# Kernel tuning notes

Measured on AMD Instinct MI355X. Metric: run time of the kernel, lower is better.

Reference implementation:

```python
import jax, jax.numpy as jnp
import numpy as np

B, N, D, H = 8, 1024, 768, 12
HD = D // H  # head_dim = 64


def setup_inputs() -> dict:
    key = jax.random.key(0)
    ks = jax.random.split(key, 7)
    s = 1.0 / np.sqrt(D)  # xavier-ish scale for weights
    return {
        "x1": jax.random.normal(ks[0], (B, N, D), dtype=jnp.float32),
        "x2": jax.random.normal(ks[1], (B, N, D), dtype=jnp.float32),
        "Wq": jax.random.normal(ks[2], (D, D), dtype=jnp.float32) * s,
        "Wk": jax.random.normal(ks[3], (D, D), dtype=jnp.float32) * s,
        "Wv": jax.random.normal(ks[4], (D, D), dtype=jnp.float32) * s,
        "Wo": jax.random.normal(ks[5], (D, D), dtype=jnp.float32) * s,
        "bo": jnp.zeros((D,), dtype=jnp.float32),
    }


def _heads(x):
    # (B, N, D) -> (B, H, N, HD)
    return x.reshape(B, -1, H, HD).transpose(0, 2, 1, 3)


def reference(x1, x2, Wq, Wk, Wv, Wo, bo):
    scale = 1.0 / jnp.sqrt(jnp.asarray(HD, x1.dtype))
    q1 = _heads(x1 @ Wq.T)               # (B,H,N,HD)
    k1 = _heads(x1 @ Wk.T)
    v1 = _heads(x1 @ Wv.T)
    k2 = _heads(x2 @ Wk.T)
    v2 = _heads(x2 @ Wv.T)
    kc = jnp.concatenate([k1, k2], axis=2)   # (B,H,2N,HD)
    vc = jnp.concatenate([v1, v2], axis=2)
    attn = jnp.einsum('bhnd,bhmd->bhnm', q1, kc) * scale  # (B,H,N,2N)
    attn = jax.nn.softmax(attn, axis=-1)
    out = jnp.einsum('bhnm,bhmd->bhnd', attn, vc)          # (B,H,N,HD)
    out = out.transpose(0, 2, 1, 3).reshape(B, N, D)
    return out @ Wo.T + bo
```

## Files before the change

### kernel.cpp

```cpp
#include <hip/hip_runtime.h>


typedef __bf16 bf16x8 __attribute__((ext_vector_type(8)));
typedef float  f32x4  __attribute__((ext_vector_type(4)));
typedef unsigned int u32x4 __attribute__((ext_vector_type(4)));
typedef short  s16x4  __attribute__((ext_vector_type(4)));
typedef short  s16x8  __attribute__((ext_vector_type(8)));

__device__ __forceinline__ unsigned short bf16bits(float f) {
    return __builtin_bit_cast(unsigned short, (__bf16)f);
}
__device__ __forceinline__ unsigned pk2(float a, float b) {
    return (unsigned)bf16bits(a) | ((unsigned)bf16bits(b) << 16);
}
__device__ __forceinline__ bf16x8 asbf(u32x4 v) {
    return __builtin_bit_cast(bf16x8, v);
}
__device__ __forceinline__ float fexp2(float x) {
#if __has_builtin(__builtin_amdgcn_exp2f)
    return __builtin_amdgcn_exp2f(x);
#else
    return exp2f(x);
#endif
}
__device__ __forceinline__ float frcp(float x) {
#if __has_builtin(__builtin_amdgcn_rcpf)
    return __builtin_amdgcn_rcpf(x);
#else
    return 1.0f / x;
#endif
}

#define MFMA32(a, b, c) __builtin_amdgcn_mfma_f32_16x16x32_bf16((a), (b), (c), 0, 0, 0)

__global__ __launch_bounds__(256) void convert_all(
    const float* __restrict__ x1, const float* __restrict__ x2,
    const float* __restrict__ Wq, const float* __restrict__ Wk,
    const float* __restrict__ Wv, const float* __restrict__ Wo,
    unsigned short* __restrict__ x1b, unsigned short* __restrict__ x2b,
    unsigned short* __restrict__ Wcat, unsigned short* __restrict__ Wob)
{
    const float* src; unsigned short* dst; int n4;
    switch (blockIdx.y) {
        case 0:  src = x1; dst = x1b;            n4 = 1572864; break;
        case 1:  src = x2; dst = x2b;            n4 = 1572864; break;
        case 2:  src = Wq; dst = Wcat;           n4 = 147456;  break;
        case 3:  src = Wk; dst = Wcat +  589824; n4 = 147456;  break;
        case 4:  src = Wv; dst = Wcat + 1179648; n4 = 147456;  break;
        default: src = Wo; dst = Wob;            n4 = 147456;  break;
    }
    int i = blockIdx.x * 256 + threadIdx.x;
    if (i >= n4) return;
    float4 v = ((const float4*)src)[i];
    unsigned* o32 = (unsigned*)(dst + (size_t)i * 4);
    o32[0] = pk2(v.x, v.y);
    o32[1] = pk2(v.z, v.w);
}

template<int MODE>
__global__ __launch_bounds__(256) void gemm_qkv(
    const unsigned short* __restrict__ A1, const unsigned short* __restrict__ A2,
    const unsigned short* __restrict__ Wcat,
    unsigned short* __restrict__ dQ, unsigned short* __restrict__ dK,
    unsigned short* __restrict__ dV, float* __restrict__ dO,
    const float* __restrict__ bias)
{
    __shared__ u32x4 smA[2048];
    __shared__ u32x4 smB[2048];

    const int tid  = threadIdx.x;
    const int lane = tid & 63;
    const int l15  = lane & 15;
    const int g    = lane >> 4;
    const int wid  = tid >> 6;
    const int rb   = blockIdx.x;
    const int jb   = blockIdx.y;
    const int wr   = (wid >> 1) * 64;
    const int wc   = (wid & 1) * 64;

    const bool br2 = (MODE == 0) && (jb >= 18);
    const unsigned short* A  = br2 ? A2 : A1;
    const unsigned short* Bw = br2 ? (Wcat + 589824) : Wcat;
    const int jcol = br2 ? (jb - 18) : jb;

    f32x4 acc[4][4] = {};

#define GSTAGE(KT, BO)                                                               \
    {                                                                                \
        int kt_ = (KT);                                                              \
        _Pragma("unroll")                                                            \
        for (int c_ = 0; c_ < 4; ++c_) {                                             \
            int i_   = (wid + c_ * 4) * 64 + lane;                                   \
            int row_ = i_ >> 3;                                                      \
            int gs_  = (i_ & 7) ^ (row_ & 7);                                        \
            const unsigned short* sa = A +                                           \
                (size_t)(rb * 128 + row_) * 768 + kt_ * 64 + gs_ * 8;                \
            __builtin_amdgcn_global_load_lds(                                        \
                (const __attribute__((address_space(1))) void*)sa,                   \
                (__attribute__((address_space(3))) void*)(smA + (BO) + (wid + c_ * 4) * 64), \
                16, 0, 0);                                                           \
            const unsigned short* sb = Bw +                                          \
                (size_t)(jcol * 128 + row_) * 768 + kt_ * 64 + gs_ * 8;              \
            __builtin_amdgcn_global_load_lds(                                        \
                (const __attribute__((address_space(1))) void*)sb,                   \
                (__attribute__((address_space(3))) void*)(smB + (BO) + (wid + c_ * 4) * 64), \
                16, 0, 0);                                                           \
        }                                                                            \
    }

    GSTAGE(0, 0)

    for (int kt = 0; kt < 12; ++kt) {
        __builtin_amdgcn_s_barrier();
        if (kt < 11) {
            GSTAGE(kt + 1, ((kt + 1) & 1) << 10)
            asm volatile("s_waitcnt vmcnt(8)" ::: "memory");
        } else {
            asm volatile("s_waitcnt vmcnt(0)" ::: "memory");
        }
        __builtin_amdgcn_s_barrier();
        __builtin_amdgcn_sched_barrier(0);

        const u32x4* bA = smA + ((kt & 1) << 10);
        const u32x4* bB = smB + ((kt & 1) << 10);

#pragma unroll
        for (int kk = 0; kk < 2; ++kk) {
            bf16x8 af[4], bfr[4];
#pragma unroll
            for (int m = 0; m < 4; ++m) {
                int row = wr + m * 16 + l15;
                af[m] = asbf(bA[row * 8 + ((kk * 4 + g) ^ (row & 7))]);
            }
#pragma unroll
            for (int n = 0; n < 4; ++n) {
                int row = wc + n * 16 + l15;
                bfr[n] = asbf(bB[row * 8 + ((kk * 4 + g) ^ (row & 7))]);
            }
#pragma unroll
            for (int m = 0; m < 4; ++m)
#pragma unroll
                for (int n = 0; n < 4; ++n)
                    acc[m][n] = MFMA32(af[m], bfr[n], acc[m][n]);
        }
    }
#undef GSTAGE

    const int rloc = wr + g * 4;
    const int cloc = wc + l15;
    const int seg  = jcol / 6;
#pragma unroll
    for (int m = 0; m < 4; ++m) {
#pragma unroll
        for (int n = 0; n < 4; ++n) {
            int r0 = rb * 128 + rloc + m * 16;
            int c  = jcol * 128 + cloc + n * 16;
            if constexpr (MODE == 2) {
#pragma unroll
                for (int reg = 0; reg < 4; ++reg)
                    dO[(size_t)(r0 + reg) * 768 + c] = acc[m][n][reg] + bias[c];
            } else {
                int b = r0 >> 10, nn = r0 & 1023;
                int cl = c - seg * 768;
                int h = cl >> 6, hd = cl & 63;
                int segq = br2 ? seg + 3 : seg;
                if (segq == 0) {
#pragma unroll
                    for (int reg = 0; reg < 4; ++reg)
                        dQ[((size_t)(b * 12 + h) * 1024 + nn + reg) * 64 + hd] =
                            bf16bits(acc[m][n][reg] * 0.18033688f);
                } else if (segq == 1 || segq == 3) {
                    size_t koff = (segq == 3) ? 1024 : 0;
#pragma unroll
                    for (int reg = 0; reg < 4; ++reg)
                        dK[((size_t)(b * 12 + h) * 2048 + koff + nn + reg) * 64 + hd] =
                            bf16bits(acc[m][n][reg]);
                } else {
                    size_t koff = (segq == 4) ? 1024 : 0;
                    uint2 w;
                    w.x = pk2(acc[m][n][0], acc[m][n][1]);
                    w.y = pk2(acc[m][n][2], acc[m][n][3]);
                    *(uint2*)(dV + ((size_t)(b * 12 + h) * 64 + hd) * 2048 +
                              koff + nn) = w;
                }
            }
        }
    }
}

__global__ __launch_bounds__(256, 3) void attn_k(
    const unsigned short* __restrict__ Q, const unsigned short* __restrict__ K,
    const unsigned short* __restrict__ Vt, unsigned short* __restrict__ AO)
{
    __shared__ u32x4 sK[1536];
    __shared__ u32x4 sV[1536];

    const int tid  = threadIdx.x;
    const int lane = tid & 63;
    const int g    = lane >> 4;
    const int l15  = lane & 15;
    const int wid  = tid >> 6;
    const int bh   = blockIdx.x;
    const int q0   = blockIdx.y * 128;

    const unsigned short* Qh = Q  + (size_t)bh * (1024 * 64);
    const unsigned short* Kh = K  + (size_t)bh * (2048 * 64);
    const unsigned short* Vh = Vt + (size_t)bh * (64 * 2048);

    bf16x8 qf[2][2];
#pragma unroll
    for (int m = 0; m < 2; ++m)
#pragma unroll
        for (int kk = 0; kk < 2; ++kk)
            qf[m][kk] = *(const bf16x8*)(Qh +
                (size_t)(q0 + wid * 32 + m * 16 + l15) * 64 + kk * 32 + g * 8);

    f32x4 o[4][2] = {};
    float lr0 = 0.f, lr1 = 0.f;

#define STAGE_TILE(T, DOFF)                                                          \
    {                                                                                \
        int t_ = (T);                                                                \
        _Pragma("unroll")                                                            \
        for (int c_ = 0; c_ < 2; ++c_) {                                             \
            int i_   = (wid + c_ * 4) * 64 + lane;                                   \
            int row_ = i_ >> 3;                                                      \
            int gsK_ = (i_ & 7) ^ ((row_ & 3) | ((row_ >> 1) & 4));                  \
            int gsV_ = (i_ & 7) ^ (row_ & 7);                                        \
            const unsigned short* srcK_ = Kh + ((size_t)t_ * 64 + row_) * 64 + gsK_ * 8; \
            __builtin_amdgcn_global_load_lds(                                        \
                (const __attribute__((address_space(1))) void*)srcK_,               \
                (__attribute__((address_space(3))) void*)(sK + (DOFF) + (wid + c_ * 4) * 64), \
                16, 0, 0);                                                           \
            const unsigned short* srcV_ = Vh + (size_t)row_ * 2048 + t_ * 64 + gsV_ * 8; \
            __builtin_amdgcn_global_load_lds(                                        \
                (const __attribute__((address_space(1))) void*)srcV_,               \
                (__attribute__((address_space(3))) void*)(sV + (DOFF) + (wid + c_ * 4) * 64), \
                16, 0, 0);                                                           \
        }                                                                            \
    }

    STAGE_TILE(0, 0)
    STAGE_TILE(1, 512)

    for (int t = 0; t < 32; ++t) {
        if (t < 31) { asm volatile("s_waitcnt vmcnt(4)" ::: "memory"); }
        else        { asm volatile("s_waitcnt vmcnt(0)" ::: "memory"); }
        __builtin_amdgcn_s_barrier();
        if (t < 30) {
            STAGE_TILE(t + 2, ((t + 2) % 3) * 512)
        }
        __builtin_amdgcn_sched_barrier(0);

        const u32x4* sKb = sK + (t % 3) * 512;
        const u32x4* sVb = sV + (t % 3) * 512;

        f32x4 s[4][2] = {};
        __builtin_amdgcn_s_setprio(1);
#pragma unroll
        for (int kk = 0; kk < 2; ++kk) {
            bf16x8 kf[4];
#pragma unroll
            for (int n = 0; n < 4; ++n) {
                int rowp = ((n & 1) << 5) + ((l15 >> 2) << 3) +
                           (((n >> 1) & 1) << 2) + (l15 & 3);
                kf[n] = asbf(sKb[rowp * 8 + ((kk * 4 + g) ^ (l15 & 7))]);
            }
#pragma unroll
            for (int n = 0; n < 4; ++n)
#pragma unroll
                for (int m = 0; m < 2; ++m)
                    s[n][m] = MFMA32(kf[n], qf[m][kk], s[n][m]);
        }
        __builtin_amdgcn_s_setprio(0);

        float sum0 = 0.f, sum1 = 0.f;
        s16x4 p16[4][2];
#pragma unroll
        for (int n = 0; n < 4; ++n) {
            float p00 = fexp2(s[n][0][0]), p01 = fexp2(s[n][0][1]);
            float p02 = fexp2(s[n][0][2]), p03 = fexp2(s[n][0][3]);
            float p10 = fexp2(s[n][1][0]), p11 = fexp2(s[n][1][1]);
            float p12 = fexp2(s[n][1][2]), p13 = fexp2(s[n][1][3]);
            sum0 += (p00 + p01) + (p02 + p03);
            sum1 += (p10 + p11) + (p12 + p13);
            p16[n][0] = (s16x4){ (short)bf16bits(p00), (short)bf16bits(p01),
                                 (short)bf16bits(p02), (short)bf16bits(p03) };
            p16[n][1] = (s16x4){ (short)bf16bits(p10), (short)bf16bits(p11),
                                 (short)bf16bits(p12), (short)bf16bits(p13) };
        }
        lr0 += sum0; lr1 += sum1;

        __builtin_amdgcn_s_setprio(1);
#pragma unroll
        for (int kk = 0; kk < 2; ++kk) {
            bf16x8 pf[2];
#pragma unroll
            for (int m = 0; m < 2; ++m)
                pf[m] = __builtin_bit_cast(bf16x8,
                    __builtin_shufflevector(p16[kk][m], p16[kk + 2][m],
                                            0, 1, 2, 3, 4, 5, 6, 7));
#pragma unroll
            for (int v = 0; v < 4; ++v) {
                int row = v * 16 + l15;
                bf16x8 vf = asbf(sVb[row * 8 + ((kk * 4 + g) ^ (row & 7))]);
#pragma unroll
                for (int m = 0; m < 2; ++m)
                    o[v][m] = MFMA32(vf, pf[m], o[v][m]);
            }
        }
        __builtin_amdgcn_s_setprio(0);
    }

    lr0 += __shfl_xor(lr0, 16); lr0 += __shfl_xor(lr0, 32);
    lr1 += __shfl_xor(lr1, 16); lr1 += __shfl_xor(lr1, 32);
    const int b = bh / 12, h = bh % 12;
    float rl0 = frcp(lr0), rl1 = frcp(lr1);
#pragma unroll
    for (int m = 0; m < 2; ++m) {
        float rl = m ? rl1 : rl0;
        int q = q0 + wid * 32 + m * 16 + l15;
        unsigned short* dst = AO + (size_t)(b * 1024 + q) * 768 + h * 64 + g * 4;
#pragma unroll
        for (int v = 0; v < 4; ++v) {
            uint2 w;
            w.x = pk2(o[v][m][0] * rl, o[v][m][1] * rl);
            w.y = pk2(o[v][m][2] * rl, o[v][m][3] * rl);
            *(uint2*)(dst + v * 16) = w;
        }
    }
#undef STAGE_TILE
}

extern "C" void kernel_launch(void* const* d_in, const int* in_sizes, int n_in,
                              void* d_out, int out_size, void* d_ws, size_t ws_size,
                              hipStream_t stream)
{
    const float* x1 = (const float*)d_in[0];
    const float* x2 = (const float*)d_in[1];
    const float* Wq = (const float*)d_in[2];
    const float* Wk = (const float*)d_in[3];
    const float* Wv = (const float*)d_in[4];
    const float* Wo = (const float*)d_in[5];
    const float* bo = (const float*)d_in[6];

    unsigned short* Wcat = (unsigned short*)d_ws;
    unsigned short* Wob  = Wcat + 1769472;
    unsigned short* x1b  = Wob  + 589824;
    unsigned short* x2b  = x1b  + 6291456;
    unsigned short* Qb   = x2b  + 6291456;
    unsigned short* Kc   = Qb   + 6291456;
    unsigned short* Vt   = Kc   + 12582912;
    unsigned short* AO   = x1b;

    convert_all<<<dim3(6144, 6), 256, 0, stream>>>(x1, x2, Wq, Wk, Wv, Wo,
                                                   x1b, x2b, Wcat, Wob);

    gemm_qkv<0><<<dim3(64, 30), 256, 0, stream>>>(x1b, x2b, Wcat,
                                                  Qb, Kc, Vt, nullptr, nullptr);

    attn_k<<<dim3(96, 8), 256, 0, stream>>>(Qb, Kc, Vt, AO);

    gemm_qkv<2><<<dim3(64, 6), 256, 0, stream>>>(AO, nullptr, Wob,
                                                 nullptr, nullptr, nullptr,
                                                 (float*)d_out, bo);
}
```

Before: 159.7 us.

## Replace QKV projection GEMM with 256x256-tile, 8-wave double-buffered kernel

```diff
diff --git a/kernel.cpp b/kernel.cpp
--- a/kernel.cpp
+++ b/kernel.cpp
@@ -5,7 +5,6 @@
 typedef float  f32x4  __attribute__((ext_vector_type(4)));
 typedef unsigned int u32x4 __attribute__((ext_vector_type(4)));
 typedef short  s16x4  __attribute__((ext_vector_type(4)));
-typedef short  s16x8  __attribute__((ext_vector_type(8)));
 
 __device__ __forceinline__ unsigned short bf16bits(float f) {
     return __builtin_bit_cast(unsigned short, (__bf16)f);
@@ -57,13 +56,182 @@
     o32[1] = pk2(v.z, v.w);
 }
 
-template<int MODE>
-__global__ __launch_bounds__(256) void gemm_qkv(
+__global__ __launch_bounds__(512, 2) void gemm256(
     const unsigned short* __restrict__ A1, const unsigned short* __restrict__ A2,
     const unsigned short* __restrict__ Wcat,
     unsigned short* __restrict__ dQ, unsigned short* __restrict__ dK,
-    unsigned short* __restrict__ dV, float* __restrict__ dO,
-    const float* __restrict__ bias)
+    unsigned short* __restrict__ dV)
+{
+    __shared__ u32x4 smA[2][2048];
+    __shared__ u32x4 smB[2][2048];
+
+    const int tid  = threadIdx.x;
+    const int lane = tid & 63;
+    const int l15  = lane & 15;
+    const int g    = lane >> 4;
+    const int wid  = tid >> 6;
+    const int wm   = wid >> 2;
+    const int wn   = wid & 3;
+    const int rb   = blockIdx.x;
+    const int jb   = blockIdx.y;
+
+    const bool br2 = (jb >= 9);
+    const unsigned short* A  = br2 ? A2 : A1;
+    const unsigned short* Bw = br2 ? (Wcat + 589824) : Wcat;
+    const int jcol = br2 ? (jb - 9) : jb;
+
+    f32x4 acc[8][4] = {};
+
+#define GSTAGE256(KT, BO)                                                            \
+    {                                                                                \
+        int kt_ = (KT);                                                              \
+        _Pragma("unroll")                                                            \
+        for (int c_ = 0; c_ < 4; ++c_) {                                             \
+            int i_   = c_ * 512 + tid;                                               \
+            int row_ = i_ >> 3;                                                      \
+            int gs_  = (i_ & 7) ^ (row_ & 7);                                        \
+            const unsigned short* sa = A +                                           \
+                (size_t)(rb * 256 + row_) * 768 + kt_ * 64 + gs_ * 8;                \
+            __builtin_amdgcn_global_load_lds(                                        \
+                (const __attribute__((address_space(1))) void*)sa,                   \
+                (__attribute__((address_space(3))) void*)(smA[BO] + c_ * 512 + wid * 64), \
+                16, 0, 0);                                                           \
+            const unsigned short* sb = Bw +                                          \
+                (size_t)(jcol * 256 + row_) * 768 + kt_ * 64 + gs_ * 8;              \
+            __builtin_amdgcn_global_load_lds(                                        \
+                (const __attribute__((address_space(1))) void*)sb,                   \
+                (__attribute__((address_space(3))) void*)(smB[BO] + c_ * 512 + wid * 64), \
+                16, 0, 0);                                                           \
+        }                                                                            \
+    }
+
+    GSTAGE256(0, 0)
+    asm volatile("s_waitcnt vmcnt(0)" ::: "memory");
+    __builtin_amdgcn_s_barrier();
+
+    for (int kt = 0; kt < 12; ++kt) {
+        const int bufc = kt & 1;
+        const u32x4* bA = smA[bufc];
+        const u32x4* bB = smB[bufc];
+        bf16x8 af[4], bfr[4];
+
+        if (kt < 11) GSTAGE256(kt + 1, bufc ^ 1)
+#pragma unroll
+        for (int n = 0; n < 4; ++n) {
+            int row = wn * 64 + n * 16 + l15;
+            bfr[n] = asbf(bB[row * 8 + (g ^ (row & 7))]);
+        }
+#pragma unroll
+        for (int m = 0; m < 4; ++m) {
+            int row = wm * 128 + m * 16 + l15;
+            af[m] = asbf(bA[row * 8 + (g ^ (row & 7))]);
+        }
+        __builtin_amdgcn_s_barrier();
+        __builtin_amdgcn_sched_barrier(0);
+        __builtin_amdgcn_s_setprio(1);
+#pragma unroll
+        for (int m = 0; m < 4; ++m)
+#pragma unroll
+            for (int n = 0; n < 4; ++n)
+                acc[m][n] = MFMA32(af[m], bfr[n], acc[m][n]);
+        __builtin_amdgcn_s_setprio(0);
+        __builtin_amdgcn_s_barrier();
+
+#pragma unroll
+        for (int m = 0; m < 4; ++m) {
+            int row = wm * 128 + 64 + m * 16 + l15;
+            af[m] = asbf(bA[row * 8 + (g ^ (row & 7))]);
+        }
+        __builtin_amdgcn_s_barrier();
+        __builtin_amdgcn_sched_barrier(0);
+        __builtin_amdgcn_s_setprio(1);
+#pragma unroll
+        for (int m = 0; m < 4; ++m)
+#pragma unroll
+            for (int n = 0; n < 4; ++n)
+                acc[4 + m][n] = MFMA32(af[m], bfr[n], acc[4 + m][n]);
+        __builtin_amdgcn_s_setprio(0);
+        __builtin_amdgcn_s_barrier();
+
+#pragma unroll
+        for (int n = 0; n < 4; ++n) {
+            int row = wn * 64 + n * 16 + l15;
+            bfr[n] = asbf(bB[row * 8 + ((4 + g) ^ (row & 7))]);
+        }
+#pragma unroll
+        for (int m = 0; m < 4; ++m) {
+            int row = wm * 128 + m * 16 + l15;
+            af[m] = asbf(bA[row * 8 + ((4 + g) ^ (row & 7))]);
+        }
+        __builtin_amdgcn_s_barrier();
+        __builtin_amdgcn_sched_barrier(0);
+        __builtin_amdgcn_s_setprio(1);
+#pragma unroll
+        for (int m = 0; m < 4; ++m)
+#pragma unroll
+            for (int n = 0; n < 4; ++n)
+                acc[m][n] = MFMA32(af[m], bfr[n], acc[m][n]);
+        __builtin_amdgcn_s_setprio(0);
+        __builtin_amdgcn_s_barrier();
+
+#pragma unroll
+        for (int m = 0; m < 4; ++m) {
+            int row = wm * 128 + 64 + m * 16 + l15;
+            af[m] = asbf(bA[row * 8 + ((4 + g) ^ (row & 7))]);
+        }
+        __builtin_amdgcn_s_barrier();
+        __builtin_amdgcn_sched_barrier(0);
+        __builtin_amdgcn_s_setprio(1);
+#pragma unroll
+        for (int m = 0; m < 4; ++m)
+#pragma unroll
+            for (int n = 0; n < 4; ++n)
+                acc[4 + m][n] = MFMA32(af[m], bfr[n], acc[4 + m][n]);
+        __builtin_amdgcn_s_setprio(0);
+        asm volatile("s_waitcnt vmcnt(0)" ::: "memory");
+        __builtin_amdgcn_s_barrier();
+    }
+#undef GSTAGE256
+
+    const int rloc = wm * 128 + g * 4;
+    const int cloc = wn * 64 + l15;
+    const int seg  = jcol / 3;
+    const int segq = br2 ? seg + 3 : seg;
+    const int cseg = (jcol - seg * 3) * 256;
+#pragma unroll
+    for (int mf = 0; mf < 8; ++mf) {
+#pragma unroll
+        for (int n = 0; n < 4; ++n) {
+            int r0 = rb * 256 + rloc + mf * 16;
+            int cl = cseg + cloc + n * 16;
+            int b = r0 >> 10, nn = r0 & 1023;
+            int h = cl >> 6, hd = cl & 63;
+            if (segq == 0) {
+#pragma unroll
+                for (int reg = 0; reg < 4; ++reg)
+                    dQ[((size_t)(b * 12 + h) * 1024 + nn + reg) * 64 + hd] =
+                        bf16bits(acc[mf][n][reg] * 0.18033688f);
+            } else if (segq == 1 || segq == 3) {
+                size_t koff = (segq == 3) ? 1024 : 0;
+#pragma unroll
+                for (int reg = 0; reg < 4; ++reg)
+                    dK[((size_t)(b * 12 + h) * 2048 + koff + nn + reg) * 64 + hd] =
+                        bf16bits(acc[mf][n][reg]);
+            } else {
+                size_t koff = (segq == 4) ? 1024 : 0;
+                uint2 w;
+                w.x = pk2(acc[mf][n][0], acc[mf][n][1]);
+                w.y = pk2(acc[mf][n][2], acc[mf][n][3]);
+                *(uint2*)(dV + ((size_t)(b * 12 + h) * 64 + hd) * 2048 +
+                          koff + nn) = w;
+            }
+        }
+    }
+}
+
+__global__ __launch_bounds__(256) void gemm_out(
+    const unsigned short* __restrict__ A, const unsigned short* __restrict__ Bw,
+    float* __restrict__ dO, const float* __restrict__ bias)
 {
     __shared__ u32x4 smA[2048];
     __shared__ u32x4 smB[2048];
@@ -77,11 +245,6 @@
     const int jb   = blockIdx.y;
     const int wr   = (wid >> 1) * 64;
     const int wc   = (wid & 1) * 64;
-
-    const bool br2 = (MODE == 0) && (jb >= 18);
-    const unsigned short* A  = br2 ? A2 : A1;
-    const unsigned short* Bw = br2 ? (Wcat + 589824) : Wcat;
-    const int jcol = br2 ? (jb - 18) : jb;
 
     f32x4 acc[4][4] = {};
 
@@ -100,7 +263,7 @@
                 (__attribute__((address_space(3))) void*)(smA + (BO) + (wid + c_ * 4) * 64), \
                 16, 0, 0);                                                           \
             const unsigned short* sb = Bw +                                          \
-                (size_t)(jcol * 128 + row_) * 768 + kt_ * 64 + gs_ * 8;              \
+                (size_t)(jb * 128 + row_) * 768 + kt_ * 64 + gs_ * 8;                \
             __builtin_amdgcn_global_load_lds(                                        \
                 (const __attribute__((address_space(1))) void*)sb,                   \
                 (__attribute__((address_space(3))) void*)(smB + (BO) + (wid + c_ * 4) * 64), \
@@ -148,44 +311,16 @@
 
     const int rloc = wr + g * 4;
     const int cloc = wc + l15;
-    const int seg  = jcol / 6;
-#pragma unroll
-    for (int m = 0; m < 4; ++m) {
+#pragma unroll
+    for (int m = 0; m < 4; ++m)
 #pragma unroll
         for (int n = 0; n < 4; ++n) {
             int r0 = rb * 128 + rloc + m * 16;
-            int c  = jcol * 128 + cloc + n * 16;
-            if constexpr (MODE == 2) {
-#pragma unroll
-                for (int reg = 0; reg < 4; ++reg)
-                    dO[(size_t)(r0 + reg) * 768 + c] = acc[m][n][reg] + bias[c];
-            } else {
-                int b = r0 >> 10, nn = r0 & 1023;
-                int cl = c - seg * 768;
-                int h = cl >> 6, hd = cl & 63;
-                int segq = br2 ? seg + 3 : seg;
-                if (segq == 0) {
-#pragma unroll
-                    for (int reg = 0; reg < 4; ++reg)
-                        dQ[((size_t)(b * 12 + h) * 1024 + nn + reg) * 64 + hd] =
-                            bf16bits(acc[m][n][reg] * 0.18033688f);
-                } else if (segq == 1 || segq == 3) {
-                    size_t koff = (segq == 3) ? 1024 : 0;
-#pragma unroll
-                    for (int reg = 0; reg < 4; ++reg)
-                        dK[((size_t)(b * 12 + h) * 2048 + koff + nn + reg) * 64 + hd] =
-                            bf16bits(acc[m][n][reg]);
-                } else {
-                    size_t koff = (segq == 4) ? 1024 : 0;
-                    uint2 w;
-                    w.x = pk2(acc[m][n][0], acc[m][n][1]);
-                    w.y = pk2(acc[m][n][2], acc[m][n][3]);
-                    *(uint2*)(dV + ((size_t)(b * 12 + h) * 64 + hd) * 2048 +
-                              koff + nn) = w;
-                }
-            }
-        }
-    }
+            int c  = jb * 128 + cloc + n * 16;
+#pragma unroll
+            for (int reg = 0; reg < 4; ++reg)
+                dO[(size_t)(r0 + reg) * 768 + c] = acc[m][n][reg] + bias[c];
+        }
 }
 
 __global__ __launch_bounds__(256, 3) void attn_k(
@@ -356,12 +491,9 @@
     convert_all<<<dim3(6144, 6), 256, 0, stream>>>(x1, x2, Wq, Wk, Wv, Wo,
                                                    x1b, x2b, Wcat, Wob);
 
-    gemm_qkv<0><<<dim3(64, 30), 256, 0, stream>>>(x1b, x2b, Wcat,
-                                                  Qb, Kc, Vt, nullptr, nullptr);
+    gemm256<<<dim3(32, 15), 512, 0, stream>>>(x1b, x2b, Wcat, Qb, Kc, Vt);
 
     attn_k<<<dim3(96, 8), 256, 0, stream>>>(Qb, Kc, Vt, AO);
 
-    gemm_qkv<2><<<dim3(64, 6), 256, 0, stream>>>(AO, nullptr, Wob,
-                                                 nullptr, nullptr, nullptr,
-                                                 (float*)d_out, bo);
-}
+    gemm_out<<<dim3(64, 6), 256, 0, stream>>>(AO, Wob, (float*)d_out, bo);
+}
```

Result: slower. 164.3 us (+2.9%).

## Double attention query tile per block to 256 rows and split out-projection GEMM

Applied to the files above, without the earlier changes.

```diff
diff --git a/kernel.cpp b/kernel.cpp
--- a/kernel.cpp
+++ b/kernel.cpp
@@ -5,7 +5,6 @@
 typedef float  f32x4  __attribute__((ext_vector_type(4)));
 typedef unsigned int u32x4 __attribute__((ext_vector_type(4)));
 typedef short  s16x4  __attribute__((ext_vector_type(4)));
-typedef short  s16x8  __attribute__((ext_vector_type(8)));
 
 __device__ __forceinline__ unsigned short bf16bits(float f) {
     return __builtin_bit_cast(unsigned short, (__bf16)f);
@@ -62,8 +61,7 @@
     const unsigned short* __restrict__ A1, const unsigned short* __restrict__ A2,
     const unsigned short* __restrict__ Wcat,
     unsigned short* __restrict__ dQ, unsigned short* __restrict__ dK,
-    unsigned short* __restrict__ dV, float* __restrict__ dO,
-    const float* __restrict__ bias)
+    unsigned short* __restrict__ dV)
 {
     __shared__ u32x4 smA[2048];
     __shared__ u32x4 smB[2048];
@@ -78,7 +76,7 @@
     const int wr   = (wid >> 1) * 64;
     const int wc   = (wid & 1) * 64;
 
-    const bool br2 = (MODE == 0) && (jb >= 18);
+    const bool br2 = (jb >= 18);
     const unsigned short* A  = br2 ? A2 : A1;
     const unsigned short* Bw = br2 ? (Wcat + 589824) : Wcat;
     const int jcol = br2 ? (jb - 18) : jb;
@@ -155,40 +153,128 @@
         for (int n = 0; n < 4; ++n) {
             int r0 = rb * 128 + rloc + m * 16;
             int c  = jcol * 128 + cloc + n * 16;
-            if constexpr (MODE == 2) {
+            int b = r0 >> 10, nn = r0 & 1023;
+            int cl = c - seg * 768;
+            int h = cl >> 6, hd = cl & 63;
+            int segq = br2 ? seg + 3 : seg;
+            if (segq == 0) {
 #pragma unroll
                 for (int reg = 0; reg < 4; ++reg)
-                    dO[(size_t)(r0 + reg) * 768 + c] = acc[m][n][reg] + bias[c];
+                    dQ[((size_t)(b * 12 + h) * 1024 + nn + reg) * 64 + hd] =
+                        bf16bits(acc[m][n][reg] * 0.18033688f);
+            } else if (segq == 1 || segq == 3) {
+                size_t koff = (segq == 3) ? 1024 : 0;
+#pragma unroll
+                for (int reg = 0; reg < 4; ++reg)
+                    dK[((size_t)(b * 12 + h) * 2048 + koff + nn + reg) * 64 + hd] =
+                        bf16bits(acc[m][n][reg]);
             } else {
-                int b = r0 >> 10, nn = r0 & 1023;
-                int cl = c - seg * 768;
-                int h = cl >> 6, hd = cl & 63;
-                int segq = br2 ? seg + 3 : seg;
-                if (segq == 0) {
-#pragma unroll
-                    for (int reg = 0; reg < 4; ++reg)
-                        dQ[((size_t)(b * 12 + h) * 1024 + nn + reg) * 64 + hd] =
-                            bf16bits(acc[m][n][reg] * 0.18033688f);
-                } else if (segq == 1 || segq == 3) {
-                    size_t koff = (segq == 3) ? 1024 : 0;
-#pragma unroll
-                    for (int reg = 0; reg < 4; ++reg)
-                        dK[((size_t)(b * 12 + h) * 2048 + koff + nn + reg) * 64 + hd] =
-                            bf16bits(acc[m][n][reg]);
-                } else {
-                    size_t koff = (segq == 4) ? 1024 : 0;
-                    uint2 w;
-                    w.x = pk2(acc[m][n][0], acc[m][n][1]);
-                    w.y = pk2(acc[m][n][2], acc[m][n][3]);
-                    *(uint2*)(dV + ((size_t)(b * 12 + h) * 64 + hd) * 2048 +
-                              koff + nn) = w;
-                }
-            }
-        }
-    }
-}
-
-__global__ __launch_bounds__(256, 3) void attn_k(
+                size_t koff = (segq == 4) ? 1024 : 0;
+                uint2 w;
+                w.x = pk2(acc[m][n][0], acc[m][n][1]);
+                w.y = pk2(acc[m][n][2], acc[m][n][3]);
+                *(uint2*)(dV + ((size_t)(b * 12 + h) * 64 + hd) * 2048 +
+                          koff + nn) = w;
+            }
+        }
+    }
+}
+
+__global__ __launch_bounds__(256) void gemm_out(
+    const unsigned short* __restrict__ A, const unsigned short* __restrict__ Bw,
+    float* __restrict__ dO, const float* __restrict__ bias)
+{
+    __shared__ u32x4 smA[2048];
+    __shared__ u32x4 smB[2048];
+
+    const int tid  = threadIdx.x;
+    const int lane = tid & 63;
+    const int l15  = lane & 15;
+    const int g    = lane >> 4;
+    const int wid  = tid >> 6;
+    const int rb   = blockIdx.x;
+    const int jb   = blockIdx.y;
+    const int wr   = (wid >> 1) * 64;
+    const int wc   = (wid & 1) * 64;
+
+    f32x4 acc[4][4] = {};
+
+#define GSTAGE(KT, BO)                                                               \
+    {                                                                                \
+        int kt_ = (KT);                                                              \
+        _Pragma("unroll")                                                            \
+        for (int c_ = 0; c_ < 4; ++c_) {                                             \
+            int i_   = (wid + c_ * 4) * 64 + lane;                                   \
+            int row_ = i_ >> 3;                                                      \
+            int gs_  = (i_ & 7) ^ (row_ & 7);                                        \
+            const unsigned short* sa = A +                                           \
+                (size_t)(rb * 128 + row_) * 768 + kt_ * 64 + gs_ * 8;                \
+            __builtin_amdgcn_global_load_lds(                                        \
+                (const __attribute__((address_space(1))) void*)sa,                   \
+                (__attribute__((address_space(3))) void*)(smA + (BO) + (wid + c_ * 4) * 64), \
+                16, 0, 0);                                                           \
+            const unsigned short* sb = Bw +                                          \
+                (size_t)(jb * 128 + row_) * 768 + kt_ * 64 + gs_ * 8;                \
+            __builtin_amdgcn_global_load_lds(                                        \
+                (const __attribute__((address_space(1))) void*)sb,                   \
+                (__attribute__((address_space(3))) void*)(smB + (BO) + (wid + c_ * 4) * 64), \
+                16, 0, 0);                                                           \
+        }                                                                            \
+    }
+
+    GSTAGE(0, 0)
+
+    for (int kt = 0; kt < 12; ++kt) {
+        __builtin_amdgcn_s_barrier();
+        if (kt < 11) {
+            GSTAGE(kt + 1, ((kt + 1) & 1) << 10)
+            asm volatile("s_waitcnt vmcnt(8)" ::: "memory");
+        } else {
+            asm volatile("s_waitcnt vmcnt(0)" ::: "memory");
+        }
+        __builtin_amdgcn_s_barrier();
+        __builtin_amdgcn_sched_barrier(0);
+
+        const u32x4* bA = smA + ((kt & 1) << 10);
+        const u32x4* bB = smB + ((kt & 1) << 10);
+
+#pragma unroll
+        for (int kk = 0; kk < 2; ++kk) {
+            bf16x8 af[4], bfr[4];
+#pragma unroll
+            for (int m = 0; m < 4; ++m) {
+                int row = wr + m * 16 + l15;
+                af[m] = asbf(bA[row * 8 + ((kk * 4 + g) ^ (row & 7))]);
+            }
+#pragma unroll
+            for (int n = 0; n < 4; ++n) {
+                int row = wc + n * 16 + l15;
+                bfr[n] = asbf(bB[row * 8 + ((kk * 4 + g) ^ (row & 7))]);
+            }
+#pragma unroll
+            for (int m = 0; m < 4; ++m)
+#pragma unroll
+                for (int n = 0; n < 4; ++n)
+                    acc[m][n] = MFMA32(af[m], bfr[n], acc[m][n]);
+        }
+    }
+#undef GSTAGE
+
+    const int rloc = wr + g * 4;
+    const int cloc = wc + l15;
+#pragma unroll
+    for (int m = 0; m < 4; ++m)
+#pragma unroll
+        for (int n = 0; n < 4; ++n) {
+            int r0 = rb * 128 + rloc + m * 16;
+            int c  = jb * 128 + cloc + n * 16;
+#pragma unroll
+            for (int reg = 0; reg < 4; ++reg)
+                dO[(size_t)(r0 + reg) * 768 + c] = acc[m][n][reg] + bias[c];
+        }
+}
+
+__global__ __launch_bounds__(256, 2) void attn_k(
     const unsigned short* __restrict__ Q, const unsigned short* __restrict__ K,
     const unsigned short* __restrict__ Vt, unsigned short* __restrict__ AO)
 {
@@ -201,22 +287,22 @@
     const int l15  = lane & 15;
     const int wid  = tid >> 6;
     const int bh   = blockIdx.x;
-    const int q0   = blockIdx.y * 128;
+    const int q0   = blockIdx.y * 256;
 
     const unsigned short* Qh = Q  + (size_t)bh * (1024 * 64);
     const unsigned short* Kh = K  + (size_t)bh * (2048 * 64);
     const unsigned short* Vh = Vt + (size_t)bh * (64 * 2048);
 
-    bf16x8 qf[2][2];
-#pragma unroll
-    for (int m = 0; m < 2; ++m)
+    bf16x8 qf[4][2];
+#pragma unroll
+    for (int m = 0; m < 4; ++m)
 #pragma unroll
         for (int kk = 0; kk < 2; ++kk)
             qf[m][kk] = *(const bf16x8*)(Qh +
-                (size_t)(q0 + wid * 32 + m * 16 + l15) * 64 + kk * 32 + g * 8);
-
-    f32x4 o[4][2] = {};
-    float lr0 = 0.f, lr1 = 0.f;
+                (size_t)(q0 + wid * 64 + m * 16 + l15) * 64 + kk * 32 + g * 8);
+
+    f32x4 o[4][4] = {};
+    float lr[4] = {0.f, 0.f, 0.f, 0.f};
 
 #define STAGE_TILE(T, DOFF)                                                          \
     {                                                                                \
@@ -255,7 +341,7 @@
         const u32x4* sKb = sK + (t % 3) * 512;
         const u32x4* sVb = sV + (t % 3) * 512;
 
-        f32x4 s[4][2] = {};
+        f32x4 s[4][4] = {};
         __builtin_amdgcn_s_setprio(1);
 #pragma unroll
         for (int kk = 0; kk < 2; ++kk) {
@@ -269,34 +355,32 @@
 #pragma unroll
             for (int n = 0; n < 4; ++n)
 #pragma unroll
-                for (int m = 0; m < 2; ++m)
+                for (int m = 0; m < 4; ++m)
                     s[n][m] = MFMA32(kf[n], qf[m][kk], s[n][m]);
         }
         __builtin_amdgcn_s_setprio(0);
 
-        float sum0 = 0.f, sum1 = 0.f;
-        s16x4 p16[4][2];
-#pragma unroll
-        for (int n = 0; n < 4; ++n) {
-            float p00 = fexp2(s[n][0][0]), p01 = fexp2(s[n][0][1]);
-            float p02 = fexp2(s[n][0][2]), p03 = fexp2(s[n][0][3]);
-            float p10 = fexp2(s[n][1][0]), p11 = fexp2(s[n][1][1]);
-            float p12 = fexp2(s[n][1][2]), p13 = fexp2(s[n][1][3]);
-            sum0 += (p00 + p01) + (p02 + p03);
-            sum1 += (p10 + p11) + (p12 + p13);
-            p16[n][0] = (s16x4){ (short)bf16bits(p00), (short)bf16bits(p01),
-                                 (short)bf16bits(p02), (short)bf16bits(p03) };
-            p16[n][1] = (s16x4){ (short)bf16bits(p10), (short)bf16bits(p11),
-                                 (short)bf16bits(p12), (short)bf16bits(p13) };
-        }
-        lr0 += sum0; lr1 += sum1;
+        s16x4 p16[4][4];
+#pragma unroll
+        for (int m = 0; m < 4; ++m) {
+            float sum = 0.f;
+#pragma unroll
+            for (int n = 0; n < 4; ++n) {
+                float p0 = fexp2(s[n][m][0]), p1 = fexp2(s[n][m][1]);
+                float p2 = fexp2(s[n][m][2]), p3 = fexp2(s[n][m][3]);
+                sum += (p0 + p1) + (p2 + p3);
+                p16[n][m] = (s16x4){ (short)bf16bits(p0), (short)bf16bits(p1),
+                                     (short)bf16bits(p2), (short)bf16bits(p3) };
+            }
+            lr[m] += sum;
+        }
 
         __builtin_amdgcn_s_setprio(1);
 #pragma unroll
         for (int kk = 0; kk < 2; ++kk) {
-            bf16x8 pf[2];
-#pragma unroll
-            for (int m = 0; m < 2; ++m)
+            bf16x8 pf[4];
+#pragma unroll
+            for (int m = 0; m < 4; ++m)
                 pf[m] = __builtin_bit_cast(bf16x8,
                     __builtin_shufflevector(p16[kk][m], p16[kk + 2][m],
                                             0, 1, 2, 3, 4, 5, 6, 7));
@@ -305,21 +389,20 @@
                 int row = v * 16 + l15;
                 bf16x8 vf = asbf(sVb[row * 8 + ((kk * 4 + g) ^ (row & 7))]);
 #pragma unroll
-                for (int m = 0; m < 2; ++m)
+                for (int m = 0; m < 4; ++m)
                     o[v][m] = MFMA32(vf, pf[m], o[v][m]);
             }
         }
         __builtin_amdgcn_s_setprio(0);
     }
 
-    lr0 += __shfl_xor(lr0, 16); lr0 += __shfl_xor(lr0, 32);
-    lr1 += __shfl_xor(lr1, 16); lr1 += __shfl_xor(lr1, 32);
     const int b = bh / 12, h = bh % 12;
-    float rl0 = frcp(lr0), rl1 = frcp(lr1);
-#pragma unroll
-    for (int m = 0; m < 2; ++m) {
-        float rl = m ? rl1 : rl0;
-        int q = q0 + wid * 32 + m * 16 + l15;
+#pragma unroll
+    for (int m = 0; m < 4; ++m) {
+        float l = lr[m];
+        l += __shfl_xor(l, 16); l += __shfl_xor(l, 32);
+        float rl = frcp(l);
+        int q = q0 + wid * 64 + m * 16 + l15;
         unsigned short* dst = AO + (size_t)(b * 1024 + q) * 768 + h * 64 + g * 4;
 #pragma unroll
         for (int v = 0; v < 4; ++v) {
@@ -356,12 +439,9 @@
     convert_all<<<dim3(6144, 6), 256, 0, stream>>>(x1, x2, Wq, Wk, Wv, Wo,
                                                    x1b, x2b, Wcat, Wob);
 
-    gemm_qkv<0><<<dim3(64, 30), 256, 0, stream>>>(x1b, x2b, Wcat,
-                                                  Qb, Kc, Vt, nullptr, nullptr);
-
-    attn_k<<<dim3(96, 8), 256, 0, stream>>>(Qb, Kc, Vt, AO);
-
-    gemm_qkv<2><<<dim3(64, 6), 256, 0, stream>>>(AO, nullptr, Wob,
-                                                 nullptr, nullptr, nullptr,
-                                                 (float*)d_out, bo);
-}
+    gemm_qkv<0><<<dim3(64, 30), 256, 0, stream>>>(x1b, x2b, Wcat, Qb, Kc, Vt);
+
+    attn_k<<<dim3(96, 4), 256, 0, stream>>>(Qb, Kc, Vt, AO);
+
+    gemm_out<<<dim3(64, 6), 256, 0, stream>>>(AO, Wob, (float*)d_out, bo);
+}
```

Result: slower. 168.7 us (+5.6%).
